# Kernel tuning notes

Hardware: AMD Instinct MI355X
Metric: run time of the kernel (lower is better)

The kernel has to match this reference:

```python
import jax, jax.numpy as jnp
import numpy as np

WINDOW_SIZE = 3
STRIDE = 3
CHANNEL = 3
SIGMA = 1.5
C1 = 0.01 ** 2
C2 = 0.03 ** 2


def _make_window():
    # 1D gaussian (sigma=1.5), normalized, outer product -> 2D window, tiled per channel [C,1,ws,ws]
    ws = WINDOW_SIZE
    g = np.exp(-((np.arange(ws) - ws // 2) ** 2) / (2.0 * SIGMA ** 2))
    g = (g / g.sum()).astype(np.float32)
    w2 = np.outer(g, g)
    return jnp.asarray(np.tile(w2[None, None], (CHANNEL, 1, 1, 1)))


def _dwconv(x, w):
    # depthwise conv2d, padding=(ws-1)//2, stride=STRIDE, groups=CHANNEL
    pad = (WINDOW_SIZE - 1) // 2
    return jax.lax.conv_general_dilated(
        x, w,
        window_strides=(STRIDE, STRIDE),
        padding=[(pad, pad), (pad, pad)],
        dimension_numbers=("NCHW", "OIHW", "NCHW"),
        feature_group_count=CHANNEL,
    )


def setup_inputs() -> dict:
    key = jax.random.key(0)
    k1, k2 = jax.random.split(key)
    img1 = jax.random.uniform(k1, (16, 3, 512, 512), dtype=jnp.float32)
    img2 = jax.random.uniform(k2, (16, 3, 512, 512), dtype=jnp.float32)
    return {"img1": img1, "img2": img2, "window": _make_window()}


def reference(img1, img2, window):
    mu1 = _dwconv(img1, window)
    mu2 = _dwconv(img2, window)
    mu1_sq = mu1 * mu1
    mu2_sq = mu2 * mu2
    mu1_mu2 = mu1 * mu2
    sigma1_sq = _dwconv(img1 * img1, window) - mu1_sq
    sigma2_sq = _dwconv(img2 * img2, window) - mu2_sq
    sigma12 = _dwconv(img1 * img2, window) - mu1_mu2
    ssim_map = (2.0 * mu1_mu2 + C1) * (2.0 * sigma12 + C2) / (
        (mu1_sq + mu2_sq + C1) * (sigma1_sq + sigma2_sq + C2)
    )
    # size_average=True -> scalar mean
    return ssim_map.mean()
```

## Files before the change

kernel.cpp:

```cpp
#include <hip/hip_runtime.h>


#define HW     512
#define OHW    171
#define NPLANE 48
#define NOUT   (NPLANE * OHW * OHW)
#define NBLK   2048
#define TPB    256

__global__ __launch_bounds__(TPB) void ssim_main(
    const float* __restrict__ img1, const float* __restrict__ img2,
    const float* __restrict__ win, float* __restrict__ partial) {
  float w[9];
#pragma unroll
  for (int i = 0; i < 9; ++i) w[i] = win[i];

  const float C1 = 0.01f * 0.01f;
  const float C2 = 0.03f * 0.03f;

  float acc = 0.0f;
  for (int idx = blockIdx.x * TPB + threadIdx.x; idx < NOUT; idx += NBLK * TPB) {
    int ox = idx % OHW;
    int t  = idx / OHW;
    int oy = t % OHW;
    int p  = t / OHW;
    const float* a = img1 + (size_t)p * HW * HW;
    const float* b = img2 + (size_t)p * HW * HW;
    int ix0 = 3 * ox - 1;
    int iy0 = 3 * oy - 1;

    float s1 = 0.f, s2 = 0.f, s11 = 0.f, s22 = 0.f, s12 = 0.f;
#pragma unroll
    for (int ky = 0; ky < 3; ++ky) {
      int iy = iy0 + ky;
      if (iy < 0) continue;
      const float* ar = a + (size_t)iy * HW;
      const float* br = b + (size_t)iy * HW;
#pragma unroll
      for (int kx = 0; kx < 3; ++kx) {
        int ix = ix0 + kx;
        if (ix < 0) continue;
        float wv = w[ky * 3 + kx];
        float x = ar[ix];
        float y = br[ix];
        s1  += wv * x;
        s2  += wv * y;
        s11 += wv * x * x;
        s22 += wv * y * y;
        s12 += wv * x * y;
      }
    }
    float mu11 = s1 * s1, mu22 = s2 * s2, mu12 = s1 * s2;
    float sg1 = s11 - mu11, sg2 = s22 - mu22, sg12 = s12 - mu12;
    float num = (2.0f * mu12 + C1) * (2.0f * sg12 + C2);
    float den = (mu11 + mu22 + C1) * (sg1 + sg2 + C2);
    acc += num / den;
  }

#pragma unroll
  for (int off = 32; off > 0; off >>= 1) acc += __shfl_down(acc, off, 64);
  __shared__ float wsum[TPB / 64];
  int lane = threadIdx.x & 63, wid = threadIdx.x >> 6;
  if (lane == 0) wsum[wid] = acc;
  __syncthreads();
  if (threadIdx.x == 0) {
    float s = 0.f;
#pragma unroll
    for (int i = 0; i < TPB / 64; ++i) s += wsum[i];
    partial[blockIdx.x] = s;
  }
}

__global__ __launch_bounds__(256) void ssim_final(
    const float* __restrict__ partial, float* __restrict__ out) {
  float acc = 0.f;
  for (int i = threadIdx.x; i < NBLK; i += 256) acc += partial[i];
#pragma unroll
  for (int off = 32; off > 0; off >>= 1) acc += __shfl_down(acc, off, 64);
  __shared__ float wsum[4];
  int lane = threadIdx.x & 63, wid = threadIdx.x >> 6;
  if (lane == 0) wsum[wid] = acc;
  __syncthreads();
  if (threadIdx.x == 0) {
    float s = 0.f;
#pragma unroll
    for (int i = 0; i < 4; ++i) s += wsum[i];
    out[0] = s / (float)NOUT;
  }
}

extern "C" void kernel_launch(void* const* d_in, const int* in_sizes, int n_in,
                              void* d_out, int out_size, void* d_ws, size_t ws_size,
                              hipStream_t stream) {
  const float* img1 = (const float*)d_in[0];
  const float* img2 = (const float*)d_in[1];
  const float* win  = (const float*)d_in[2];
  float* partial = (float*)d_ws;
  float* out = (float*)d_out;

  ssim_main<<<NBLK, TPB, 0, stream>>>(img1, img2, win, partial);
  ssim_final<<<1, 256, 0, stream>>>(partial, out);
}
```

Before: 127.0 us.

## Compute four outputs per thread with float4 row loads

```diff
diff --git a/kernel.cpp b/kernel.cpp
--- a/kernel.cpp
+++ b/kernel.cpp
@@ -1,12 +1,17 @@
 #include <hip/hip_runtime.h>
 
 
-#define HW     512
-#define OHW    171
-#define NPLANE 48
-#define NOUT   (NPLANE * OHW * OHW)
-#define NBLK   2048
-#define TPB    256
+#define HW       512
+#define PLANE_SZ (HW * HW)
+#define OHW      171
+#define NPLANE   48
+#define NOUT     (NPLANE * OHW * OHW)
+#define OX4      43
+#define NGROUPS  (NPLANE * OHW * OX4)
+#define TPB      256
+#define NBLK     ((NGROUPS + TPB - 1) / TPB)
+
+typedef float f4 __attribute__((ext_vector_type(4)));
 
 __global__ __launch_bounds__(TPB) void ssim_main(
     const float* __restrict__ img1, const float* __restrict__ img2,
@@ -19,48 +24,80 @@
   const float C2 = 0.03f * 0.03f;
 
   float acc = 0.0f;
-  for (int idx = blockIdx.x * TPB + threadIdx.x; idx < NOUT; idx += NBLK * TPB) {
-    int ox = idx % OHW;
-    int t  = idx / OHW;
-    int oy = t % OHW;
-    int p  = t / OHW;
-    const float* a = img1 + (size_t)p * HW * HW;
-    const float* b = img2 + (size_t)p * HW * HW;
-    int ix0 = 3 * ox - 1;
-    int iy0 = 3 * oy - 1;
+  const int idx = blockIdx.x * TPB + threadIdx.x;
+  if (idx < NGROUPS) {
+    int ox4 = idx % OX4;
+    int t   = idx / OX4;
+    int oy  = t % OHW;
+    int p   = t / OHW;
+    const float* a = img1 + (size_t)p * PLANE_SZ;
+    const float* b = img2 + (size_t)p * PLANE_SZ;
+    const int iy0 = 3 * oy - 1;
+    const int q0  = 3 * ox4 - 1;
 
-    float s1 = 0.f, s2 = 0.f, s11 = 0.f, s22 = 0.f, s12 = 0.f;
+    float s1[4]  = {0.f, 0.f, 0.f, 0.f};
+    float s2[4]  = {0.f, 0.f, 0.f, 0.f};
+    float s11[4] = {0.f, 0.f, 0.f, 0.f};
+    float s22[4] = {0.f, 0.f, 0.f, 0.f};
+    float s12[4] = {0.f, 0.f, 0.f, 0.f};
+
 #pragma unroll
-    for (int ky = 0; ky < 3; ++ky) {
-      int iy = iy0 + ky;
-      if (iy < 0) continue;
-      const float* ar = a + (size_t)iy * HW;
-      const float* br = b + (size_t)iy * HW;
+    for (int r = 0; r < 3; ++r) {
+      const int iy = iy0 + r;
+      float xa[16], xb[16];
+      if (iy >= 0) {
+        const f4* pa = (const f4*)(a + (size_t)iy * HW);
+        const f4* pb = (const f4*)(b + (size_t)iy * HW);
 #pragma unroll
-      for (int kx = 0; kx < 3; ++kx) {
-        int ix = ix0 + kx;
-        if (ix < 0) continue;
-        float wv = w[ky * 3 + kx];
-        float x = ar[ix];
-        float y = br[ix];
-        s1  += wv * x;
-        s2  += wv * y;
-        s11 += wv * x * x;
-        s22 += wv * y * y;
-        s12 += wv * x * y;
+        for (int tq = 0; tq < 4; ++tq) {
+          const int q = q0 + tq;
+          f4 va = {0.f, 0.f, 0.f, 0.f};
+          f4 vb = {0.f, 0.f, 0.f, 0.f};
+          if (q >= 0 && q < HW / 4) { va = pa[q]; vb = pb[q]; }
+#pragma unroll
+          for (int e = 0; e < 4; ++e) { xa[4 * tq + e] = va[e]; xb[4 * tq + e] = vb[e]; }
+        }
+      } else {
+#pragma unroll
+        for (int e = 0; e < 16; ++e) { xa[e] = 0.f; xb[e] = 0.f; }
+      }
+#pragma unroll
+      for (int j = 0; j < 4; ++j) {
+#pragma unroll
+        for (int kx = 0; kx < 3; ++kx) {
+          const float wv = w[3 * r + kx];
+          const float x = xa[3 * j + 3 + kx];
+          const float y = xb[3 * j + 3 + kx];
+          s1[j]  += wv * x;
+          s2[j]  += wv * y;
+          s11[j] += wv * x * x;
+          s22[j] += wv * y * y;
+          s12[j] += wv * x * y;
+        }
       }
     }
-    float mu11 = s1 * s1, mu22 = s2 * s2, mu12 = s1 * s2;
-    float sg1 = s11 - mu11, sg2 = s22 - mu22, sg12 = s12 - mu12;
-    float num = (2.0f * mu12 + C1) * (2.0f * sg12 + C2);
-    float den = (mu11 + mu22 + C1) * (sg1 + sg2 + C2);
-    acc += num / den;
+
+    const int oxb = 4 * ox4;
+#pragma unroll
+    for (int j = 0; j < 4; ++j) {
+      if (oxb + j < OHW) {
+        const float mu11 = s1[j] * s1[j];
+        const float mu22 = s2[j] * s2[j];
+        const float mu12 = s1[j] * s2[j];
+        const float sg1  = s11[j] - mu11;
+        const float sg2  = s22[j] - mu22;
+        const float sg12 = s12[j] - mu12;
+        const float num = (2.0f * mu12 + C1) * (2.0f * sg12 + C2);
+        const float den = (mu11 + mu22 + C1) * (sg1 + sg2 + C2);
+        acc += num / den;
+      }
+    }
   }
 
 #pragma unroll
   for (int off = 32; off > 0; off >>= 1) acc += __shfl_down(acc, off, 64);
   __shared__ float wsum[TPB / 64];
-  int lane = threadIdx.x & 63, wid = threadIdx.x >> 6;
+  const int lane = threadIdx.x & 63, wid = threadIdx.x >> 6;
   if (lane == 0) wsum[wid] = acc;
   __syncthreads();
   if (threadIdx.x == 0) {
@@ -73,19 +110,19 @@
 
 __global__ __launch_bounds__(256) void ssim_final(
     const float* __restrict__ partial, float* __restrict__ out) {
-  float acc = 0.f;
-  for (int i = threadIdx.x; i < NBLK; i += 256) acc += partial[i];
+  double acc = 0.0;
+  for (int i = threadIdx.x; i < NBLK; i += 256) acc += (double)partial[i];
 #pragma unroll
   for (int off = 32; off > 0; off >>= 1) acc += __shfl_down(acc, off, 64);
-  __shared__ float wsum[4];
-  int lane = threadIdx.x & 63, wid = threadIdx.x >> 6;
+  __shared__ double wsum[4];
+  const int lane = threadIdx.x & 63, wid = threadIdx.x >> 6;
   if (lane == 0) wsum[wid] = acc;
   __syncthreads();
   if (threadIdx.x == 0) {
-    float s = 0.f;
+    double s = 0.0;
 #pragma unroll
     for (int i = 0; i < 4; ++i) s += wsum[i];
-    out[0] = s / (float)NOUT;
+    out[0] = (float)(s / (double)NOUT);
   }
 }
 
```

New measurement: 132.8 us. +4.5%, slower.
